# Kernel optimization log

Hardware: AMD Instinct MI355X
Metric: run time of the kernel (lower is better)

## Reference

```python
import jax, jax.numpy as jnp
import numpy as np

WS = 16        # window size
SHIFT = 8      # shift for odd blocks
DEPTH = 2      # number of stacked blocks
HEADS = 8
EPS = 1e-5


def window_partition(x, ws):
    # x: (B,H,W,C) -> (B*nw, ws*ws, C)
    B, H, W, C = x.shape
    x = x.reshape(B, H // ws, ws, W // ws, ws, C).transpose(0, 1, 3, 2, 4, 5)
    return x.reshape(-1, ws * ws, C)


def window_reverse(wins, ws, H, W):
    B = wins.shape[0] // ((H // ws) * (W // ws))
    x = wins.reshape(B, H // ws, W // ws, ws, ws, -1).transpose(0, 1, 3, 2, 4, 5)
    return x.reshape(B, H, W, -1)


def layernorm(x, g, b):
    m = jnp.mean(x, axis=-1, keepdims=True)
    v = jnp.mean(jnp.square(x - m), axis=-1, keepdims=True)
    return (x - m) * jax.lax.rsqrt(v + EPS) * g + b


def _make_rpi(ws):
    # Swin relative position index, shape (ws*ws, ws*ws), int32
    coords = np.stack(np.meshgrid(np.arange(ws), np.arange(ws), indexing='ij'))  # (2,ws,ws)
    coords = coords.reshape(2, -1)
    rel = coords[:, :, None] - coords[:, None, :]  # (2, n, n)
    rel = rel + (ws - 1)
    rpi = rel[0] * (2 * ws - 1) + rel[1]
    return jnp.asarray(rpi, dtype=jnp.int32)


def _make_attn_mask(H, W, ws, shift):
    # Swin shifted-window mask, shape (nw, n, n) with 0 / -100
    img = np.zeros((1, H, W, 1), dtype=np.float32)
    cnt = 0
    slices = (slice(0, -ws), slice(-ws, -shift), slice(-shift, None))
    for hs in slices:
        for wsl in slices:
            img[:, hs, wsl, :] = cnt
            cnt += 1
    mw = window_partition(jnp.asarray(img), ws).reshape(-1, ws * ws)  # (nw, n)
    mask = mw[:, None, :] - mw[:, :, None]
    return jnp.where(mask != 0, jnp.float32(-100.0), jnp.float32(0.0))


def setup_inputs() -> dict:
    key = jax.random.key(0)
    ks = jax.random.split(key, 8)
    B, H, W, C = 8, 64, 64, 256
    hid = 4 * C
    d = DEPTH
    s = 0.02
    inp = {
        'x':      jax.random.normal(ks[0], (B, H, W, C), jnp.float32),
        'ln1_g':  jnp.ones((d, C), jnp.float32),
        'ln1_b':  jnp.zeros((d, C), jnp.float32),
        'qkv_w':  jax.random.normal(ks[1], (d, C, 3 * C), jnp.float32) * s,
        'qkv_b':  jnp.zeros((d, 3 * C), jnp.float32),
        'rpb':    jax.random.normal(ks[2], (d, (2 * WS - 1) ** 2, HEADS), jnp.float32) * s,
        'proj_w': jax.random.normal(ks[3], (d, C, C), jnp.float32) * s,
        'proj_b': jnp.zeros((d, C), jnp.float32),
        'ln2_g':  jnp.ones((d, C), jnp.float32),
        'ln2_b':  jnp.zeros((d, C), jnp.float32),
        'fc1_w':  jax.random.normal(ks[4], (d, C, hid), jnp.float32) * s,
        'fc1_b':  jnp.zeros((d, hid), jnp.float32),
        'fc2_w':  jax.random.normal(ks[5], (d, hid, C), jnp.float32) * s,
        'fc2_b':  jnp.zeros((d, C), jnp.float32),
        'attn_mask': _make_attn_mask(H, W, WS, SHIFT),
        'rpi':    _make_rpi(WS),
    }
    return inp


def _forward(x, ln1_g, ln1_b, qkv_w, qkv_b, rpb, proj_w, proj_b,
             ln2_g, ln2_b, fc1_w, fc1_b, fc2_w, fc2_b, attn_mask, rpi):
    B, H, W, C = x.shape
    n = WS * WS
    hd = C // HEADS
    scale = jnp.float32(hd) ** -0.5
    for i in range(DEPTH):
        shift = SHIFT if (i % 2 == 1) else 0
        shortcut = x
        y = layernorm(x, ln1_g[i], ln1_b[i])
        if shift:
            y = jnp.roll(y, (-shift, -shift), axis=(1, 2))
        wins = window_partition(y, WS)                      # (b_, n, C)
        b_ = wins.shape[0]
        qkv = wins @ qkv_w[i] + qkv_b[i]
        qkv = qkv.reshape(b_, n, 3, HEADS, hd).transpose(2, 0, 3, 1, 4)
        q, k, v = qkv[0] * scale, qkv[1], qkv[2]            # (b_,h,n,hd)
        attn = jnp.einsum('bhnd,bhmd->bhnm', q, k)          # (b_,h,n,n)
        bias = rpb[i][rpi.reshape(-1)].reshape(n, n, HEADS).transpose(2, 0, 1)
        attn = attn + bias[None]
        if shift:
            nw = attn_mask.shape[0]
            attn = attn.reshape(B, nw, HEADS, n, n) + attn_mask[None, :, None]
            attn = attn.reshape(b_, HEADS, n, n)
        attn = jax.nn.softmax(attn, axis=-1)
        out = jnp.einsum('bhnm,bhmd->bhnd', attn, v)
        out = out.transpose(0, 2, 1, 3).reshape(b_, n, C)
        out = out @ proj_w[i] + proj_b[i]
        y = window_reverse(out, WS, H, W)
        if shift:
            y = jnp.roll(y, (shift, shift), axis=(1, 2))
        x = shortcut + y
        z = layernorm(x, ln2_g[i], ln2_b[i])
        z = jax.nn.gelu(z @ fc1_w[i] + fc1_b[i], approximate=False)
        z = z @ fc2_w[i] + fc2_b[i]
        x = x + z
    return x


def reference(x, ln1_g, ln1_b, qkv_w, qkv_b, rpb, proj_w, proj_b,
              ln2_g, ln2_b, fc1_w, fc1_b, fc2_w, fc2_b, attn_mask, rpi):
    return _forward(x, ln1_g, ln1_b, qkv_w, qkv_b, rpb, proj_w, proj_b,
                    ln2_g, ln2_b, fc1_w, fc1_b, fc2_w, fc2_b, attn_mask, rpi)
```

## Files before the change

### kernel.cpp

```cpp
#include <hip/hip_runtime.h>

typedef unsigned short u16;
typedef __attribute__((ext_vector_type(8))) short short8;
typedef __attribute__((ext_vector_type(4))) float f32x4;

#define GLDS16(gp, sp) __builtin_amdgcn_global_load_lds( \
    (const __attribute__((address_space(1))) void*)(gp),  \
    (__attribute__((address_space(3))) void*)(sp), 16, 0, 0)

__device__ __forceinline__ u16 f2bf(float f) {
  union { float f; unsigned u; } x; x.f = f;
  unsigned r = (x.u + 0x7fffu + ((x.u >> 16) & 1u)) >> 16;
  return (u16)r;
}
__device__ __forceinline__ float bf2f(u16 v) {
  union { unsigned u; float f; } x; x.u = ((unsigned)v) << 16; return x.f;
}

__global__ __launch_bounds__(256) void wswizB(const float* __restrict__ W,
                                              u16* __restrict__ Wf, int K, int N) {
  int tid = blockIdx.x * 256 + threadIdx.x;
  int Kt = K >> 5, Nt = N >> 4;
  int per = Nt * Kt * 64;
  if (tid >= 2 * per) return;
  int l = tid >= per;
  int rem = tid - l * per;
  int nb = rem / (Kt * 64);
  int rem2 = rem - nb * Kt * 64;
  int ks = rem2 >> 6, lane = rem2 & 63;
  int n = nb * 16 + (lane & 15);
  u16 o[8];
  #pragma unroll
  for (int e = 0; e < 8; ++e) {
    int k = ks * 32 + ((lane >> 4) << 3) + e;
    o[e] = f2bf(W[((size_t)l * K + k) * N + n]);
  }
  *(uint4*)(Wf + ((size_t)tid << 3)) = *(uint4*)o;
}

__global__ __launch_bounds__(256) void wswiz1(const float* __restrict__ W,
                                              u16* __restrict__ Wf) {
  int tid = blockIdx.x * 256 + threadIdx.x;
  int lane = tid & 63, nt = (tid >> 6) & 7, ks = (tid >> 9) & 7,
      hc = (tid >> 12) & 7, l = tid >> 15;
  int n = hc * 128 + nt * 16 + (lane & 15);
  u16 o[8];
  #pragma unroll
  for (int e = 0; e < 8; ++e) {
    int k = ks * 32 + ((lane >> 4) << 3) + e;
    o[e] = f2bf(W[((size_t)l * 256 + k) * 1024 + n]);
  }
  *(uint4*)(Wf + ((size_t)tid << 3)) = *(uint4*)o;
}

__global__ __launch_bounds__(256) void wswiz2(const float* __restrict__ W,
                                              u16* __restrict__ Wf) {
  int tid = blockIdx.x * 256 + threadIdx.x;
  int lane = tid & 63, nt = (tid >> 6) & 15, ks = (tid >> 10) & 3,
      hc = (tid >> 12) & 7, l = tid >> 15;
  int n = nt * 16 + (lane & 15);
  u16 o[8];
  #pragma unroll
  for (int e = 0; e < 8; ++e) {
    int k = hc * 128 + ks * 32 + ((lane >> 4) << 3) + e;
    o[e] = f2bf(W[((size_t)l * 1024 + k) * 256 + n]);
  }
  *(uint4*)(Wf + ((size_t)tid << 3)) = *(uint4*)o;
}

__global__ __launch_bounds__(256) void bias_gb(const float* __restrict__ rpb,
                                               const int* __restrict__ rpi,
                                               u16* __restrict__ biasb) {
  int tid = blockIdx.x * 256 + threadIdx.x;
  if (tid >= 131072) return;
  int l = tid >> 16, cid = tid & 65535;
  int lane = cid & 63, k = (cid >> 6) & 7, mslot = (cid >> 9) & 15, h = cid >> 13;
  u16 o[8];
  #pragma unroll
  for (int e = 0; e < 8; ++e) {
    int nt = 2 * k + (e >> 2), r = e & 3;
    int i = mslot * 16 + ((lane >> 4) << 2) + r;
    int j = nt * 16 + (lane & 15);
    int idx = rpi[i * 256 + j];
    o[e] = f2bf(rpb[((size_t)l * 961 + idx) * 8 + h]);
  }
  *(uint4*)(biasb + ((size_t)tid << 3)) = *(uint4*)o;
}

__global__ __launch_bounds__(256) void ln_part(const float* __restrict__ x,
                                               const float* __restrict__ g,
                                               const float* __restrict__ b,
                                               u16* __restrict__ out, int shift) {
  int wv = threadIdx.x >> 6, lane = threadIdx.x & 63;
  int wtok = blockIdx.x * 4 + wv;
  int w = wtok >> 8, t = wtok & 255;
  int bimg = w >> 4, wi = w & 15;
  int ph = (((wi >> 2) << 4) + (t >> 4) + shift) & 63;
  int pw = (((wi & 3) << 4) + (t & 15) + shift) & 63;
  const float4 v = *(const float4*)(x + ((size_t)((bimg * 64 + ph) * 64 + pw)) * 256 + lane * 4);
  float s = v.x + v.y + v.z + v.w;
  float sq = v.x * v.x + v.y * v.y + v.z * v.z + v.w * v.w;
  #pragma unroll
  for (int m = 1; m < 64; m <<= 1) { s += __shfl_xor(s, m, 64); sq += __shfl_xor(sq, m, 64); }
  float mean = s * (1.f / 256.f);
  float var = sq * (1.f / 256.f) - mean * mean;
  float rs = rsqrtf(var + 1e-5f);
  float4 gg = *(const float4*)(g + lane * 4);
  float4 bb = *(const float4*)(b + lane * 4);
  u16 o0 = f2bf((v.x - mean) * rs * gg.x + bb.x);
  u16 o1 = f2bf((v.y - mean) * rs * gg.y + bb.y);
  u16 o2 = f2bf((v.z - mean) * rs * gg.z + bb.z);
  u16 o3 = f2bf((v.w - mean) * rs * gg.w + bb.w);
  uint2 pk; pk.x = (unsigned)o0 | ((unsigned)o1 << 16); pk.y = (unsigned)o2 | ((unsigned)o3 << 16);
  *(uint2*)(out + (size_t)wtok * 256 + lane * 4) = pk;
}

struct EpiParams {
  const float* bias;
  u16* obf;
  float* of32;
  const float* resid;
  int shift;
  float qscale;
};

template <int EPI>
__global__ __launch_bounds__(256, 4) void gemm_bt(const u16* __restrict__ A,
                                                  const u16* __restrict__ Wf,
                                                  int M, int N, int K, EpiParams ep) {
  __shared__ u16 As[128 * 32];
  int tid = threadIdx.x;
  int n0 = blockIdx.x * 128, m0 = blockIdx.y * 128;
  int wv = tid >> 6, lane = tid & 63, quad = lane >> 4, l15 = lane & 15;
  int wm = wv & 1, wn = wv >> 1;
  int Kt = K >> 5;
  f32x4 acc[4][4] = {};

  for (int k0 = 0; k0 < K; k0 += 32) {
    #pragma unroll
    for (int it = 0; it < 2; ++it) {
      int c = it * 256 + tid;
      int r = c >> 2, kc = (c & 3) * 8;
      GLDS16(A + (size_t)(m0 + r) * K + k0 + kc, &As[c * 8]);
    }
    __syncthreads();
    short8 af[4], bf[4];
    #pragma unroll
    for (int mt = 0; mt < 4; ++mt)
      af[mt] = *(const short8*)&As[(wm * 64 + mt * 16 + l15) * 32 + quad * 8];
    #pragma unroll
    for (int nt = 0; nt < 4; ++nt) {
      size_t ntile = (size_t)(blockIdx.x * 8 + wn * 4 + nt);
      bf[nt] = *(const short8*)(Wf + ((ntile * Kt + (k0 >> 5)) * 64 + lane) * 8);
    }
    #pragma unroll
    for (int mt = 0; mt < 4; ++mt)
      #pragma unroll
      for (int nt = 0; nt < 4; ++nt)
        acc[mt][nt] = __builtin_amdgcn_mfma_f32_16x16x32_bf16(af[mt], bf[nt], acc[mt][nt], 0, 0, 0);
    __syncthreads();
  }

  #pragma unroll
  for (int mt = 0; mt < 4; ++mt) {
    #pragma unroll
    for (int nt = 0; nt < 4; ++nt) {
      #pragma unroll
      for (int r = 0; r < 4; ++r) {
        int grow = m0 + wm * 64 + mt * 16 + quad * 4 + r;
        int gcol = n0 + wn * 64 + nt * 16 + l15;
        float v = acc[mt][nt][r] + ep.bias[gcol];
        if constexpr (EPI == 0) {
          if (gcol < 256) v *= ep.qscale;
          ep.obf[(size_t)grow * N + gcol] = f2bf(v);
        } else {
          int w_ = grow >> 8, t = grow & 255, wi = w_ & 15;
          int ph = (((wi >> 2) << 4) + (t >> 4) + ep.shift) & 63;
          int pw = (((wi & 3) << 4) + (t & 15) + ep.shift) & 63;
          size_t pix = (size_t)(((w_ >> 4) * 64 + ph) * 64 + pw);
          ep.of32[pix * 256 + gcol] = ep.resid[pix * 256 + gcol] + v;
        }
      }
    }
  }
}

__global__ __launch_bounds__(512, 4) void fused_mlp(const float* __restrict__ xin,
                                                    const float* __restrict__ g,
                                                    const float* __restrict__ b,
                                                    const u16* __restrict__ W1f,
                                                    const u16* __restrict__ W2f,
                                                    const float* __restrict__ b1p,
                                                    const float* __restrict__ b2p,
                                                    float* __restrict__ out) {
  __shared__ u16 Zs[64 * 264];
  __shared__ u16 Hs[2][64 * 136];
  int tid = threadIdx.x, wv = tid >> 6, lane = tid & 63;
  int quad = lane >> 4, l15 = lane & 15;
  int m0 = blockIdx.x * 64;

  float4 gg = *(const float4*)(g + lane * 4);
  float4 bb = *(const float4*)(b + lane * 4);
  #pragma unroll
  for (int rr = 0; rr < 8; ++rr) {
    int row = wv * 8 + rr;
    const float4 v = *(const float4*)(xin + (size_t)(m0 + row) * 256 + lane * 4);
    float s = v.x + v.y + v.z + v.w;
    float sq = v.x * v.x + v.y * v.y + v.z * v.z + v.w * v.w;
    #pragma unroll
    for (int m = 1; m < 64; m <<= 1) { s += __shfl_xor(s, m, 64); sq += __shfl_xor(sq, m, 64); }
    float mean = s * (1.f / 256.f);
    float var = sq * (1.f / 256.f) - mean * mean;
    float rs = rsqrtf(var + 1e-5f);
    u16 o0 = f2bf((v.x - mean) * rs * gg.x + bb.x);
    u16 o1 = f2bf((v.y - mean) * rs * gg.y + bb.y);
    u16 o2 = f2bf((v.z - mean) * rs * gg.z + bb.z);
    u16 o3 = f2bf((v.w - mean) * rs * gg.w + bb.w);
    uint2 pk; pk.x = (unsigned)o0 | ((unsigned)o1 << 16); pk.y = (unsigned)o2 | ((unsigned)o3 << 16);
    *(uint2*)&Zs[row * 264 + lane * 4] = pk;
  }
  __syncthreads();

  f32x4 acc2[4][2];
  #pragma unroll
  for (int nt = 0; nt < 2; ++nt) {
    float b2 = b2p[wv * 32 + nt * 16 + l15];
    #pragma unroll
    for (int mt = 0; mt < 4; ++mt)
      #pragma unroll
      for (int r = 0; r < 4; ++r) acc2[mt][nt][r] = b2;
  }

  for (int hc = 0; hc < 8; ++hc) {
    f32x4 acc1[4];
    {
      float b1 = b1p[hc * 128 + wv * 16 + l15];
      #pragma unroll
      for (int mt = 0; mt < 4; ++mt)
        #pragma unroll
        for (int r = 0; r < 4; ++r) acc1[mt][r] = b1;
    }
    #pragma unroll
    for (int ks = 0; ks < 8; ++ks) {
      short8 bf = *(const short8*)(W1f + ((((size_t)hc * 8 + ks) * 8 + wv) * 64 + lane) * 8);
      #pragma unroll
      for (int mt = 0; mt < 4; ++mt) {
        short8 af = *(const short8*)&Zs[(mt * 16 + l15) * 264 + ks * 32 + quad * 8];
        acc1[mt] = __builtin_amdgcn_mfma_f32_16x16x32_bf16(af, bf, acc1[mt], 0, 0, 0);
      }
    }
    u16* hs = &Hs[hc & 1][0];
    #pragma unroll
    for (int mt = 0; mt < 4; ++mt)
      #pragma unroll
      for (int r = 0; r < 4; ++r) {
        float v = acc1[mt][r];
        float inner = v * (1.f + 0.044715f * v * v);
        float e = __expf(-1.5957691216057308f * inner);
        float gl = v * __builtin_amdgcn_rcpf(1.f + e);
        hs[(mt * 16 + quad * 4 + r) * 136 + wv * 16 + l15] = f2bf(gl);
      }
    __syncthreads();
    #pragma unroll
    for (int ks = 0; ks < 4; ++ks) {
      short8 bf2[2];
      #pragma unroll
      for (int nt = 0; nt < 2; ++nt)
        bf2[nt] = *(const short8*)(W2f + ((((size_t)hc * 4 + ks) * 16 + wv * 2 + nt) * 64 + lane) * 8);
      #pragma unroll
      for (int mt = 0; mt < 4; ++mt) {
        short8 af2 = *(const short8*)&hs[(mt * 16 + l15) * 136 + ks * 32 + quad * 8];
        #pragma unroll
        for (int nt = 0; nt < 2; ++nt)
          acc2[mt][nt] = __builtin_amdgcn_mfma_f32_16x16x32_bf16(af2, bf2[nt], acc2[mt][nt], 0, 0, 0);
      }
    }
  }

  #pragma unroll
  for (int mt = 0; mt < 4; ++mt)
    #pragma unroll
    for (int nt = 0; nt < 2; ++nt)
      #pragma unroll
      for (int r = 0; r < 4; ++r) {
        size_t idx = (size_t)(m0 + mt * 16 + quad * 4 + r) * 256 + wv * 32 + nt * 16 + l15;
        out[idx] = xin[idx] + acc2[mt][nt][r];
      }
}

__global__ __launch_bounds__(256, 4) void attn_v3(const u16* __restrict__ qkv,
                                                  const u16* __restrict__ biasb,
                                                  int layer, u16* __restrict__ aout) {
  __shared__ u16 Klds[256 * 32];
  __shared__ u16 Vt[32 * 264];
  __shared__ u16 Plds[4][16 * 40];
  int bid = blockIdx.x;
  int lw = ((bid & 7) << 7) | (bid >> 3);
  int w = lw >> 3, h = lw & 7;
  int tid = threadIdx.x;

  {
    const uint4* kp = (const uint4*)(qkv + ((size_t)(w * 256 + tid)) * 768 + 256 + h * 32);
    uint4* kd = (uint4*)&Klds[tid * 32];
    kd[0] = kp[0]; kd[1] = kp[1]; kd[2] = kp[2]; kd[3] = kp[3];
    const uint4* vp = (const uint4*)(qkv + ((size_t)(w * 256 + tid)) * 768 + 512 + h * 32);
    u16 vt[32];
    *(uint4*)&vt[0]  = vp[0];
    *(uint4*)&vt[8]  = vp[1];
    *(uint4*)&vt[16] = vp[2];
    *(uint4*)&vt[24] = vp[3];
    #pragma unroll
    for (int d = 0; d < 32; ++d) Vt[d * 264 + tid] = vt[d];
  }
  __syncthreads();

  int wv = tid >> 6, lane = tid & 63, quad = lane >> 4, l15 = lane & 15;
  int wi = w & 15, wr = wi >> 2, wc = wi & 3;
  const bool masked = (layer != 0) && (wr == 3 || wc == 3);
  int rcj = (wc == 3) ? (l15 < 8 ? 1 : 2) : 0;

  #pragma unroll
  for (int mt = 0; mt < 4; ++mt) {
    int mslot = wv * 4 + mt;
    int m0 = mslot * 16;
    short8 aq = *(const short8*)(qkv + ((size_t)(w * 256 + m0 + l15)) * 768 + h * 32 + quad * 8);
    const u16* bmt = biasb + ((size_t)layer << 19) + ((size_t)h << 16) + (size_t)mslot * 4096;
    f32x4 c[16];
    #pragma unroll
    for (int k = 0; k < 8; ++k) {
      short8 bv = *(const short8*)(bmt + k * 512 + lane * 8);
      #pragma unroll
      for (int r = 0; r < 4; ++r) {
        c[2 * k][r]     = bf2f((u16)bv[r]);
        c[2 * k + 1][r] = bf2f((u16)bv[4 + r]);
      }
    }
    #pragma unroll
    for (int nt = 0; nt < 16; ++nt) {
      short8 bk = *(const short8*)&Klds[(nt * 16 + l15) * 32 + quad * 8];
      c[nt] = __builtin_amdgcn_mfma_f32_16x16x32_bf16(aq, bk, c[nt], 0, 0, 0);
    }
    if (masked) {
      int regi = ((wr == 3) ? (mslot < 8 ? 1 : 2) : 0) * 3 +
                 ((wc == 3) ? (quad < 2 ? 1 : 2) : 0);
      #pragma unroll
      for (int nt = 0; nt < 16; ++nt) {
        int regj = ((wr == 3) ? (nt < 8 ? 1 : 2) : 0) * 3 + rcj;
        float madd = (regi != regj) ? -100.f : 0.f;
        #pragma unroll
        for (int r = 0; r < 4; ++r) c[nt][r] += madd;
      }
    }
    float pm[4] = {-1e30f, -1e30f, -1e30f, -1e30f};
    #pragma unroll
    for (int nt = 0; nt < 16; ++nt)
      #pragma unroll
      for (int r = 0; r < 4; ++r) pm[r] = fmaxf(pm[r], c[nt][r]);
    #pragma unroll
    for (int r = 0; r < 4; ++r) {
      pm[r] = fmaxf(pm[r], __shfl_xor(pm[r], 1, 64));
      pm[r] = fmaxf(pm[r], __shfl_xor(pm[r], 2, 64));
      pm[r] = fmaxf(pm[r], __shfl_xor(pm[r], 4, 64));
      pm[r] = fmaxf(pm[r], __shfl_xor(pm[r], 8, 64));
    }
    float psum[4] = {0.f, 0.f, 0.f, 0.f};
    #pragma unroll
    for (int nt = 0; nt < 16; ++nt)
      #pragma unroll
      for (int r = 0; r < 4; ++r) {
        float e = __expf(c[nt][r] - pm[r]);
        c[nt][r] = e;
        psum[r] += e;
      }
    #pragma unroll
    for (int r = 0; r < 4; ++r) {
      psum[r] += __shfl_xor(psum[r], 1, 64);
      psum[r] += __shfl_xor(psum[r], 2, 64);
      psum[r] += __shfl_xor(psum[r], 4, 64);
      psum[r] += __shfl_xor(psum[r], 8, 64);
    }
    f32x4 o0 = {0.f, 0.f, 0.f, 0.f}, o1 = {0.f, 0.f, 0.f, 0.f};
    #pragma unroll
    for (int kk = 0; kk < 8; ++kk) {
      #pragma unroll
      for (int r = 0; r < 4; ++r) {
        Plds[wv][(quad * 4 + r) * 40 + l15] = f2bf(c[2 * kk][r]);
        Plds[wv][(quad * 4 + r) * 40 + 16 + l15] = f2bf(c[2 * kk + 1][r]);
      }
      short8 ap = *(const short8*)&Plds[wv][l15 * 40 + quad * 8];
      short8 bv0 = *(const short8*)&Vt[l15 * 264 + kk * 32 + quad * 8];
      short8 bv1 = *(const short8*)&Vt[(16 + l15) * 264 + kk * 32 + quad * 8];
      o0 = __builtin_amdgcn_mfma_f32_16x16x32_bf16(ap, bv0, o0, 0, 0, 0);
      o1 = __builtin_amdgcn_mfma_f32_16x16x32_bf16(ap, bv1, o1, 0, 0, 0);
    }
    #pragma unroll
    for (int r = 0; r < 4; ++r) {
      float inv = 1.f / psum[r];
      size_t row = (size_t)(w * 256 + m0 + quad * 4 + r);
      aout[row * 256 + h * 32 + l15] = f2bf(o0[r] * inv);
      aout[row * 256 + h * 32 + 16 + l15] = f2bf(o1[r] * inv);
    }
  }
}

extern "C" void kernel_launch(void* const* d_in, const int* in_sizes, int n_in,
                              void* d_out, int out_size, void* d_ws, size_t ws_size,
                              hipStream_t stream) {
  const float* x      = (const float*)d_in[0];
  const float* ln1_g  = (const float*)d_in[1];
  const float* ln1_b  = (const float*)d_in[2];
  const float* qkv_w  = (const float*)d_in[3];
  const float* qkv_b  = (const float*)d_in[4];
  const float* rpb    = (const float*)d_in[5];
  const float* proj_w = (const float*)d_in[6];
  const float* proj_b = (const float*)d_in[7];
  const float* ln2_g  = (const float*)d_in[8];
  const float* ln2_b  = (const float*)d_in[9];
  const float* fc1_w  = (const float*)d_in[10];
  const float* fc1_b  = (const float*)d_in[11];
  const float* fc2_w  = (const float*)d_in[12];
  const float* fc2_b  = (const float*)d_in[13];
  const int*   rpi    = (const int*)d_in[15];

  char* ws = (char*)d_ws;
  size_t off = 0;
  auto alloc = [&](size_t bytes) { void* p = ws + off; off += (bytes + 255) & ~(size_t)255; return p; };
  float* x_cur   = (float*)alloc((size_t)32768 * 256 * 4);
  u16* sbuf      = (u16*)alloc((size_t)32768 * 256 * 2);
  u16* qkvb      = (u16*)alloc((size_t)32768 * 768 * 2);
  u16* biasb     = (u16*)alloc((size_t)2 * 8 * 65536 * 2);
  u16* qkvF      = (u16*)alloc((size_t)2 * 196608 * 2);
  u16* projF     = (u16*)alloc((size_t)2 * 65536 * 2);
  u16* W1f       = (u16*)alloc((size_t)2 * 262144 * 2);
  u16* W2f       = (u16*)alloc((size_t)2 * 262144 * 2);

  wswizB<<<192, 256, 0, stream>>>(qkv_w, qkvF, 256, 768);
  wswizB<<<64, 256, 0, stream>>>(proj_w, projF, 256, 256);
  wswiz1<<<256, 256, 0, stream>>>(fc1_w, W1f);
  wswiz2<<<256, 256, 0, stream>>>(fc2_w, W2f);
  bias_gb<<<512, 256, 0, stream>>>(rpb, rpi, biasb);

  for (int i = 0; i < 2; ++i) {
    int shift = i ? 8 : 0;
    const float* xin = i ? x_cur : x;

    ln_part<<<8192, 256, 0, stream>>>(xin, ln1_g + i * 256, ln1_b + i * 256, sbuf, shift);

    EpiParams ep{};
    ep.bias = qkv_b + i * 768; ep.obf = qkvb; ep.qscale = 0.17677669529663687f;
    gemm_bt<0><<<dim3(6, 256), 256, 0, stream>>>(sbuf, qkvF + (size_t)i * 196608, 32768, 768, 256, ep);

    attn_v3<<<1024, 256, 0, stream>>>(qkvb, biasb, i, sbuf);

    ep = EpiParams{};
    ep.bias = proj_b + i * 256; ep.of32 = x_cur; ep.resid = xin; ep.shift = shift;
    gemm_bt<2><<<dim3(2, 256), 256, 0, stream>>>(sbuf, projF + (size_t)i * 65536, 32768, 256, 256, ep);

    fused_mlp<<<512, 512, 0, stream>>>(x_cur, ln2_g + i * 256, ln2_b + i * 256,
                                       W1f + (size_t)i * 262144, W2f + (size_t)i * 262144,
                                       fc1_b + i * 1024, fc2_b + i * 256,
                                       (i == 1) ? (float*)d_out : x_cur);
  }
}
```

Measured before the change: 424.6 us.

## Load full K=256 A tile into LDS once and use 512-thread blocks

```diff
diff --git a/kernel.cpp b/kernel.cpp
--- a/kernel.cpp
+++ b/kernel.cpp
@@ -125,50 +125,50 @@
 };
 
 template <int EPI>
-__global__ __launch_bounds__(256, 4) void gemm_bt(const u16* __restrict__ A,
+__global__ __launch_bounds__(512, 2) void gemm_fk(const u16* __restrict__ A,
                                                   const u16* __restrict__ Wf,
-                                                  int M, int N, int K, EpiParams ep) {
-  __shared__ u16 As[128 * 32];
+                                                  int N, EpiParams ep) {
+  __shared__ u16 As[8][128][32];
   int tid = threadIdx.x;
   int n0 = blockIdx.x * 128, m0 = blockIdx.y * 128;
   int wv = tid >> 6, lane = tid & 63, quad = lane >> 4, l15 = lane & 15;
   int wm = wv & 1, wn = wv >> 1;
-  int Kt = K >> 5;
-  f32x4 acc[4][4] = {};
-
-  for (int k0 = 0; k0 < K; k0 += 32) {
-    #pragma unroll
-    for (int it = 0; it < 2; ++it) {
-      int c = it * 256 + tid;
-      int r = c >> 2, kc = (c & 3) * 8;
-      GLDS16(A + (size_t)(m0 + r) * K + k0 + kc, &As[c * 8]);
-    }
-    __syncthreads();
-    short8 af[4], bf[4];
-    #pragma unroll
-    for (int mt = 0; mt < 4; ++mt)
-      af[mt] = *(const short8*)&As[(wm * 64 + mt * 16 + l15) * 32 + quad * 8];
-    #pragma unroll
-    for (int nt = 0; nt < 4; ++nt) {
-      size_t ntile = (size_t)(blockIdx.x * 8 + wn * 4 + nt);
-      bf[nt] = *(const short8*)(Wf + ((ntile * Kt + (k0 >> 5)) * 64 + lane) * 8);
-    }
-    #pragma unroll
-    for (int mt = 0; mt < 4; ++mt)
-      #pragma unroll
-      for (int nt = 0; nt < 4; ++nt)
-        acc[mt][nt] = __builtin_amdgcn_mfma_f32_16x16x32_bf16(af[mt], bf[nt], acc[mt][nt], 0, 0, 0);
-    __syncthreads();
+
+  #pragma unroll
+  for (int i = 0; i < 8; ++i) {
+    int c = i * 512 + tid;
+    int kb = c >> 9, rc = c & 511;
+    int row = rc >> 2, kc = (rc & 3) * 8;
+    GLDS16(A + (size_t)(m0 + row) * 256 + kb * 32 + kc, &As[kb][row][kc]);
+  }
+  __syncthreads();
+
+  f32x4 acc[4][2] = {};
+  #pragma unroll
+  for (int kb = 0; kb < 8; ++kb) {
+    short8 bf[2];
+    #pragma unroll
+    for (int nt = 0; nt < 2; ++nt) {
+      size_t ntile = (size_t)(blockIdx.x * 8 + wn * 2 + nt);
+      bf[nt] = *(const short8*)(Wf + ((ntile * 8 + kb) * 64 + lane) * 8);
+    }
+    #pragma unroll
+    for (int mt = 0; mt < 4; ++mt) {
+      short8 af = *(const short8*)&As[kb][wm * 64 + mt * 16 + l15][quad * 8];
+      #pragma unroll
+      for (int nt = 0; nt < 2; ++nt)
+        acc[mt][nt] = __builtin_amdgcn_mfma_f32_16x16x32_bf16(af, bf[nt], acc[mt][nt], 0, 0, 0);
+    }
   }
 
   #pragma unroll
   for (int mt = 0; mt < 4; ++mt) {
     #pragma unroll
-    for (int nt = 0; nt < 4; ++nt) {
+    for (int nt = 0; nt < 2; ++nt) {
       #pragma unroll
       for (int r = 0; r < 4; ++r) {
         int grow = m0 + wm * 64 + mt * 16 + quad * 4 + r;
-        int gcol = n0 + wn * 64 + nt * 16 + l15;
+        int gcol = n0 + wn * 32 + nt * 16 + l15;
         float v = acc[mt][nt][r] + ep.bias[gcol];
         if constexpr (EPI == 0) {
           if (gcol < 256) v *= ep.qscale;
@@ -448,13 +448,13 @@
 
     EpiParams ep{};
     ep.bias = qkv_b + i * 768; ep.obf = qkvb; ep.qscale = 0.17677669529663687f;
-    gemm_bt<0><<<dim3(6, 256), 256, 0, stream>>>(sbuf, qkvF + (size_t)i * 196608, 32768, 768, 256, ep);
+    gemm_fk<0><<<dim3(6, 256), 512, 0, stream>>>(sbuf, qkvF + (size_t)i * 196608, 768, ep);
 
     attn_v3<<<1024, 256, 0, stream>>>(qkvb, biasb, i, sbuf);
 
     ep = EpiParams{};
     ep.bias = proj_b + i * 256; ep.of32 = x_cur; ep.resid = xin; ep.shift = shift;
-    gemm_bt<2><<<dim3(2, 256), 256, 0, stream>>>(sbuf, projF + (size_t)i * 65536, 32768, 256, 256, ep);
+    gemm_fk<2><<<dim3(2, 256), 512, 0, stream>>>(sbuf, projF + (size_t)i * 65536, 256, ep);
 
     fused_mlp<<<512, 512, 0, stream>>>(x_cur, ln2_g + i * 256, ln2_b + i * 256,
                                        W1f + (size_t)i * 262144, W2f + (size_t)i * 262144,
```

Result: no change. 423.6 us (-0.2%).
